# Kernel tuning notes

Hardware: AMD Instinct MI355X
Metric: run time of the kernel (lower is better)

## Reference

```python
import jax, jax.numpy as jnp
from jax import lax
import numpy as np

COST_CLASS, COST_BBOX, COST_GIOU = 2.0, 5.0, 2.0
ALPHA, GAMMA, OTA_K = 0.25, 2.0, 5
EXPANDED_STRIDES = 32.0
DEG = 180.0 / np.pi


def _make_corners(key, prefix):
    k1, k2, k3, k4, k5 = jax.random.split(key, 5)
    cx = jax.random.uniform(k1, prefix, minval=0.0, maxval=512.0)
    cy = jax.random.uniform(k2, prefix, minval=0.0, maxval=512.0)
    w = jax.random.uniform(k3, prefix, minval=8.0, maxval=128.0)
    h = jax.random.uniform(k4, prefix, minval=8.0, maxval=128.0)
    ang = jax.random.uniform(k5, prefix, minval=0.0, maxval=np.pi)
    offs = jnp.array([[-0.5, -0.5], [0.5, -0.5], [0.5, 0.5], [-0.5, 0.5]], jnp.float32)
    wh = jnp.stack([w, h], -1)[..., None, :]          # [..., 1, 2]
    pts = offs * wh                                    # [..., 4, 2]
    c, s = jnp.cos(ang)[..., None], jnp.sin(ang)[..., None]
    rx = pts[..., 0] * c - pts[..., 1] * s + cx[..., None]
    ry = pts[..., 0] * s + pts[..., 1] * c + cy[..., None]
    return jnp.stack([rx, ry], -1).reshape(prefix + (8,))


def setup_inputs() -> dict:
    key = jax.random.key(0)
    k1, k2, k3, k4 = jax.random.split(key, 4)
    B, Q, G, C = 16, 4096, 128, 80
    return {
        "pred_logits": jax.random.normal(k1, (B, Q, C), jnp.float32),
        "pred_boxes": _make_corners(k2, (B, Q)),
        "gt_boxes": _make_corners(k3, (B, G)),
        "gt_labels": jax.random.randint(k4, (B, G), 0, C),
    }


def corners_to_cxcywha(c):  # [N,8] -> [N,5]
    xc = (c[:, 0] + c[:, 2] + c[:, 4] + c[:, 6]) / 4
    yc = (c[:, 1] + c[:, 3] + c[:, 5] + c[:, 7]) / 4
    w = jnp.sqrt((c[:, 0] - c[:, 2]) ** 2 + (c[:, 1] - c[:, 3]) ** 2)
    h = jnp.sqrt((c[:, 2] - c[:, 4]) ** 2 + (c[:, 3] - c[:, 5]) ** 2)
    ang = jnp.arctan2(c[:, 3] - c[:, 1], c[:, 2] - c[:, 0]) * DEG
    return jnp.stack([xc, yc, w, h, ang], 1)


def _aabb(b5):
    cx, cy, w, h = b5[:, 0], b5[:, 1], b5[:, 2], b5[:, 3]
    return jnp.stack([cx - w / 2, cy - h / 2, cx + w / 2, cy + h / 2], 1)


def pairwise_iou(b1, b2):
    a, b = _aabb(b1), _aabb(b2)
    lt = jnp.maximum(a[:, None, :2], b[None, :, :2])
    rb = jnp.minimum(a[:, None, 2:], b[None, :, 2:])
    wh = jnp.clip(rb - lt, 0.0)
    inter = wh[..., 0] * wh[..., 1]
    area1 = (a[:, 2] - a[:, 0]) * (a[:, 3] - a[:, 1])
    area2 = (b[:, 2] - b[:, 0]) * (b[:, 3] - b[:, 1])
    return inter / (area1[:, None] + area2[None, :] - inter + 1e-8)


def pairwise_diou(b1, b2):
    iou = pairwise_iou(b1, b2)
    a, b = _aabb(b1), _aabb(b2)
    enc = jnp.maximum(a[:, None, 2:], b[None, :, 2:]) - jnp.minimum(a[:, None, :2], b[None, :, :2])
    c2 = (enc ** 2).sum(-1) + 1e-8
    d2 = ((b1[:, None, :2] - b2[None, :, :2]) ** 2).sum(-1)
    return iou - d2 / c2


def get_in_boxes_info(boxes, gts):
    bc = boxes.reshape(-1, 4, 2).mean(1)   # [Q,2]
    gp = gts.reshape(-1, 4, 2)             # [G,4,2]
    gc = gp.mean(1)                        # [G,2]
    cdist = jnp.sqrt(((bc[:, None] - gc[None]) ** 2).sum(-1))  # [Q,G]
    v1 = gp[:, 1] - gp[:, 0]
    v2 = gp[:, 2] - gp[:, 0]
    gt_area = jnp.abs(v1[:, 0] * v2[:, 1] - v1[:, 1] * v2[:, 0]) / 2
    diag = jnp.sqrt(((gp.max(1) - gp.min(1)) ** 2).sum(-1))
    radius = diag / EXPANDED_STRIDES
    in_boxes = cdist <= (gt_area / radius)[None, :]
    in_centers = cdist <= radius[None, :]
    return in_boxes.any(1), in_boxes & in_centers


def _dedup(cost, m):
    multi = m.sum(1) > 1
    onehot = jax.nn.one_hot(jnp.argmin(cost, 1), cost.shape[1], dtype=m.dtype)
    return jnp.where(multi[:, None], onehot, m)


def _match_single(logits, pboxes, gboxes, glabels):
    Q, G = pboxes.shape[0], gboxes.shape[0]
    prob = jax.nn.sigmoid(logits)
    fg_mask, _ = get_in_boxes_info(pboxes, gboxes)
    p5, g5 = corners_to_cxcywha(pboxes), corners_to_cxcywha(gboxes)
    ious = pairwise_iou(p5, g5)
    neg = (1 - ALPHA) * prob ** GAMMA * -jnp.log(1 - prob + 1e-8)
    pos = ALPHA * (1 - prob) ** GAMMA * -jnp.log(prob + 1e-8)
    cost_class = (pos - neg)[:, glabels]                         # [Q,G]
    cost_bbox = jnp.abs(pboxes[:, None] - gboxes[None]).sum(-1)  # L1 cdist on corners
    cost_giou = -pairwise_diou(p5, g5)
    # NB: source has `+ self.cost_giou * -cost_giou`, i.e. +w*diou; replicated verbatim.
    cost = COST_BBOX * cost_bbox + COST_CLASS * cost_class + COST_GIOU * (-cost_giou)
    cost = cost + 10000.0 * (~fg_mask)[:, None].astype(cost.dtype)
    # dynamic-k: sum of top OTA_K ious per gt, truncated to int, min 1
    topk = lax.top_k(ious.T, OTA_K)[0]                 # [G, k]
    dyn_k = jnp.clip(topk.sum(-1).astype(jnp.int32), 1, Q)
    ranks = jnp.argsort(jnp.argsort(cost, axis=0), axis=0)  # ascending-cost rank per column
    matching = (ranks < dyn_k[None, :]).astype(cost.dtype)
    matching = _dedup(cost, matching)
    # ensure every gt matched (bounded replication of the while loop)
    def cond(carry):
        c, m, it = carry
        return jnp.any(m.sum(0) == 0) & (it < G)
    def body(carry):
        c, m, it = carry
        c = c + 100000.0 * (m.sum(1) > 0)[:, None].astype(c.dtype)
        unm = m.sum(0) == 0
        amin = jnp.argmin(c, 0)                          # [G]
        hit = (jnp.arange(Q)[:, None] == amin[None, :]) & unm[None, :]
        m = jnp.where(hit, 1.0, m)
        m = _dedup(c, m)
        return (c, m, it + 1)
    _, matching, _ = lax.while_loop(cond, body, (cost, matching, jnp.int32(0)))
    return matching, cost, ious


def reference(pred_logits, pred_boxes, gt_boxes, gt_labels):
    return jax.vmap(_match_single)(pred_logits, pred_boxes, gt_boxes, gt_labels)
```

## Files before the change

kernel.cpp:

```cpp
#include <hip/hip_runtime.h>
#include <cstdint>
#include <cstddef>

#define B_ 16
#define Q_ 4096
#define G_ 128
#define C_ 80
#define QCHUNK 16
#define QBLK 64
#define CHPB (QBLK / QCHUNK)
#define NCH (Q_ / QBLK)

typedef unsigned long long u64;
#define U64MAX 0xffffffffffffffffull

__device__ __forceinline__ u64 packkey(float v, int q) {
    unsigned int bts = __float_as_uint(v);
    if (bts == 0x80000000u) bts = 0u;
    bts = (bts & 0x80000000u) ? ~bts : (bts | 0x80000000u);
    return ((u64)bts << 32) | (unsigned int)q;
}

__device__ __forceinline__ u64 umin64(u64 a, u64 b) { return a < b ? a : b; }
__device__ __forceinline__ u64 umax64(u64 a, u64 b) { return a > b ? a : b; }

__device__ __forceinline__ void merge5_desc(
    float& a0, float& a1, float& a2, float& a3, float& a4,
    float b0, float b1, float b2, float b3, float b4)
{
    const float r0 = fmaxf(a0, b0);
    const float r1 = fmaxf(fmaxf(a1, b1), fminf(a0, b0));
    const float r2 = fmaxf(fmaxf(a2, b2), fmaxf(fminf(a0, b1), fminf(a1, b0)));
    const float r3 = fmaxf(fmaxf(a3, b3),
                     fmaxf(fminf(a0, b2), fmaxf(fminf(a1, b1), fminf(a2, b0))));
    const float r4 = fmaxf(fmaxf(a4, b4),
                     fmaxf(fmaxf(fminf(a0, b3), fminf(a3, b0)),
                           fmaxf(fminf(a1, b2), fminf(a2, b1))));
    a0 = r0; a1 = r1; a2 = r2; a3 = r3; a4 = r4;
}

__device__ __forceinline__ void merge5_asc(
    u64& a0, u64& a1, u64& a2, u64& a3, u64& a4,
    u64 b0, u64 b1, u64 b2, u64 b3, u64 b4)
{
    const u64 r0 = umin64(a0, b0);
    const u64 r1 = umin64(umin64(a1, b1), umax64(a0, b0));
    const u64 r2 = umin64(umin64(a2, b2), umin64(umax64(a0, b1), umax64(a1, b0)));
    const u64 r3 = umin64(umin64(a3, b3),
                   umin64(umax64(a0, b2), umin64(umax64(a1, b1), umax64(a2, b0))));
    const u64 r4 = umin64(umin64(a4, b4),
                   umin64(umin64(umax64(a0, b3), umax64(a3, b0)),
                          umin64(umax64(a1, b2), umax64(a2, b1))));
    a0 = r0; a1 = r1; a2 = r2; a3 = r3; a4 = r4;
}

__device__ __forceinline__ float focal_cost(float x) {
    float p;
    if (x >= 0.f) { const float e = expf(-x); p = 1.f / (1.f + e); }
    else          { const float e = expf(x);  p = e / (1.f + e); }
    const float pos = 0.25f * (1.f - p) * (1.f - p) * (-logf(p + 1e-8f));
    const float neg = 0.75f * p * p * (-logf(1.f - p + 1e-8f));
    return pos - neg;
}

__device__ __forceinline__ void ins_level(float& c, int& j, float& x, int& qx) {
    const bool s  = x < c;
    const float nc = s ? x : c;
    const float nx = s ? c : x;
    const int   nj = s ? qx : j;
    const int   nq = s ? j : qx;
    c = nc; x = nx; j = nj; qx = nq;
}

__global__ __launch_bounds__(256) void fused_cost_kernel(
    const float* __restrict__ logits,
    const float* __restrict__ pboxes,
    const float* __restrict__ gboxes,
    const int*   __restrict__ glabels,
    float* __restrict__ out_cost,
    float* __restrict__ out_iou,
    float* __restrict__ piou,
    u64*   __restrict__ pcost,
    int*   __restrict__ ramin,
    int*   __restrict__ cnt)
{
    const int tid = threadIdx.x;
    const int g   = tid & 127;
    const int qh  = tid >> 7;
    const int ci  = blockIdx.x, b = blockIdx.y;

    __shared__ float pq[QCHUNK][16];
    __shared__ int   fgf[QCHUNK];
    __shared__ float lbuf[QCHUNK * 80];
    __shared__ float s_cost[QCHUNK][G_ + 1];
    __shared__ u64   khalf[G_][5];
    __shared__ float phalf[G_][5];

    if (tid < QBLK) cnt[b * Q_ + ci * QBLK + tid] = 0;

    const float4* gb4 = (const float4*)(gboxes + ((size_t)b * G_ + g) * 8);
    const float4 gA = gb4[0], gB = gb4[1];
    const float g0 = gA.x, g1 = gA.y, g2 = gA.z, g3 = gA.w;
    const float g4 = gB.x, g5 = gB.y, g6 = gB.z, g7 = gB.w;
    const float gxc = (g0 + g2 + g4 + g6) * 0.25f;
    const float gyc = (g1 + g3 + g5 + g7) * 0.25f;
    const float gw = sqrtf((g0 - g2) * (g0 - g2) + (g1 - g3) * (g1 - g3));
    const float gh = sqrtf((g2 - g4) * (g2 - g4) + (g3 - g5) * (g3 - g5));
    const float gax0 = gxc - gw * 0.5f, gay0 = gyc - gh * 0.5f;
    const float gax1 = gxc + gw * 0.5f, gay1 = gyc + gh * 0.5f;
    const float garea = (gax1 - gax0) * (gay1 - gay0);
    const float v1x = g2 - g0, v1y = g3 - g1, v2x = g4 - g0, v2y = g5 - g1;
    const float gt_area = fabsf(v1x * v2y - v1y * v2x) * 0.5f;
    const float mxx = fmaxf(fmaxf(g0, g2), fmaxf(g4, g6));
    const float mnx = fminf(fminf(g0, g2), fminf(g4, g6));
    const float mxy = fmaxf(fmaxf(g1, g3), fmaxf(g5, g7));
    const float mny = fminf(fminf(g1, g3), fminf(g5, g7));
    const float dgx = mxx - mnx, dgy = mxy - mny;
    const float radius = sqrtf(dgx * dgx + dgy * dgy) / 32.0f;
    const float thresh = gt_area / radius;
    const int lab = glabels[b * G_ + g];

    float c0 = 1e38f, c1 = 1e38f, c2 = 1e38f, c3 = 1e38f, c4 = 1e38f;
    int   j0 = 0, j1 = 0, j2 = 0, j3 = 0, j4 = 0;
    float t0 = 0.f, t1 = 0.f, t2 = 0.f, t3 = 0.f, t4 = 0.f;

    #pragma unroll 1
    for (int ch = 0; ch < CHPB; ++ch) {
        const int q0 = ci * QBLK + ch * QCHUNK;

        if (tid < 32) {
            const float4 v = ((const float4*)(pboxes + ((size_t)b * Q_ + q0) * 8))[tid];
            *(float4*)&pq[tid >> 1][(tid & 1) * 4] = v;
        }
        __syncthreads();
        if (tid < QCHUNK) {
            const float* pr = pq[tid];
            const float p0 = pr[0], p1 = pr[1], p2 = pr[2], p3 = pr[3];
            const float p4 = pr[4], p5v = pr[5], p6 = pr[6], p7 = pr[7];
            const float pxc = (p0 + p2 + p4 + p6) * 0.25f;
            const float pyc = (p1 + p3 + p5v + p7) * 0.25f;
            const float pw = sqrtf((p0 - p2) * (p0 - p2) + (p1 - p3) * (p1 - p3));
            const float ph = sqrtf((p2 - p4) * (p2 - p4) + (p3 - p5v) * (p3 - p5v));
            pq[tid][8]  = pxc;
            pq[tid][9]  = pyc;
            pq[tid][10] = pxc - pw * 0.5f;
            pq[tid][11] = pyc - ph * 0.5f;
            pq[tid][12] = pxc + pw * 0.5f;
            pq[tid][13] = pyc + ph * 0.5f;
            pq[tid][14] = pw * ph;
            fgf[tid] = 0;
        }
        __syncthreads();
        for (int j = tid; j < QCHUNK * 80; j += 256)
            lbuf[j] = focal_cost(logits[((size_t)b * Q_ + q0) * 80 + j]);

        const int lane0 = ((tid & 63) == 0);
        for (int i = 0; i < QCHUNK / 2; ++i) {
            const int ql = 2 * i + qh;
            const float dx = pq[ql][8] - gxc, dy = pq[ql][9] - gyc;
            const int in = sqrtf(dx * dx + dy * dy) <= thresh;
            const int anyin = __any(in);
            if (anyin && lane0) fgf[ql] = 1;
        }
        __syncthreads();

        int o = (b * Q_ + q0 + qh) * G_ + g;
        #pragma unroll
        for (int jj = 0; jj < 8; ++jj) {
            const int qls = 2 * jj + qh;
            const int q   = q0 + qls;
            const float4 prA = *(const float4*)&pq[qls][0];
            const float4 prB = *(const float4*)&pq[qls][4];
            const float4 prC = *(const float4*)&pq[qls][8];
            const float4 prD = *(const float4*)&pq[qls][12];
            const float p0 = prA.x, p1 = prA.y, p2 = prA.z, p3 = prA.w;
            const float p4 = prB.x, p5v = prB.y, p6 = prB.z, p7 = prB.w;
            const float pxc = prC.x, pyc = prC.y;
            const float pax0 = prC.z, pay0 = prC.w, pax1 = prD.x, pay1 = prD.y;
            const float parea = prD.z;

            const float l1 = fabsf(p0 - g0) + fabsf(p1 - g1) + fabsf(p2 - g2)
                           + fabsf(p3 - g3) + fabsf(p4 - g4) + fabsf(p5v - g5)
                           + fabsf(p6 - g6) + fabsf(p7 - g7);

            const float ltx = fmaxf(pax0, gax0), lty = fmaxf(pay0, gay0);
            const float rbx = fminf(pax1, gax1), rby = fminf(pay1, gay1);
            const float iw = fmaxf(rbx - ltx, 0.f), ih = fmaxf(rby - lty, 0.f);
            const float inter = iw * ih;
            const float iou = inter / (parea + garea - inter + 1e-8f);

            const float ew = fmaxf(pax1, gax1) - fminf(pax0, gax0);
            const float eh = fmaxf(pay1, gay1) - fminf(pay0, gay0);
            const float cc2 = ew * ew + eh * eh + 1e-8f;
            const float dx = pxc - gxc, dy = pyc - gyc;
            const float diou = iou - (dx * dx + dy * dy) / cc2;

            const float cclass = lbuf[qls * 80 + lab];
            const float cost = 5.f * l1 + 2.f * cclass + 2.f * diou
                             + (fgf[qls] ? 0.f : 10000.f);

            out_cost[o] = cost;
            out_iou[o]  = iou;
            o += 2 * G_;
            s_cost[qls][g] = cost;

            { float x = cost; int qx = q;
              ins_level(c0, j0, x, qx);
              ins_level(c1, j1, x, qx);
              ins_level(c2, j2, x, qx);
              ins_level(c3, j3, x, qx);
              ins_level(c4, j4, x, qx); }
            { float y = iou, m;
              m = fmaxf(t0, y); y = fminf(t0, y); t0 = m;
              m = fmaxf(t1, y); y = fminf(t1, y); t1 = m;
              m = fmaxf(t2, y); y = fminf(t2, y); t2 = m;
              m = fmaxf(t3, y); y = fminf(t3, y); t3 = m;
              t4 = fmaxf(t4, y); }
        }
        __syncthreads();

        {
            const int part = tid & 15;
            const int row  = tid >> 4;
            float v = 1e38f; int mg = 0x7fffffff;
            #pragma unroll
            for (int j = 0; j < 8; ++j) {
                const int gg = part + 16 * j;
                const float c = s_cost[row][gg];
                if (c < v) { v = c; mg = gg; }
            }
            #pragma unroll
            for (int off = 1; off < 16; off <<= 1) {
                const float ov = __shfl_xor(v, off);
                const int   og = __shfl_xor(mg, off);
                if (ov < v || (ov == v && og < mg)) { v = ov; mg = og; }
            }
            if (part == 0) ramin[b * Q_ + q0 + row] = mg;
        }
    }

    if (qh == 1) {
        khalf[g][0] = packkey(c0, j0); khalf[g][1] = packkey(c1, j1);
        khalf[g][2] = packkey(c2, j2); khalf[g][3] = packkey(c3, j3);
        khalf[g][4] = packkey(c4, j4);
        phalf[g][0] = t0; phalf[g][1] = t1; phalf[g][2] = t2;
        phalf[g][3] = t3; phalf[g][4] = t4;
    }
    __syncthreads();
    if (qh == 0) {
        u64 a0 = packkey(c0, j0), a1 = packkey(c1, j1), a2 = packkey(c2, j2),
            a3 = packkey(c3, j3), a4 = packkey(c4, j4);
        merge5_asc(a0, a1, a2, a3, a4,
                   khalf[g][0], khalf[g][1], khalf[g][2], khalf[g][3], khalf[g][4]);
        merge5_desc(t0, t1, t2, t3, t4,
                    phalf[g][0], phalf[g][1], phalf[g][2], phalf[g][3], phalf[g][4]);
        const size_t pbase = (((size_t)b * NCH + ci) * G_ + g) * 5;
        piou[pbase + 0] = t0; piou[pbase + 1] = t1; piou[pbase + 2] = t2;
        piou[pbase + 3] = t3; piou[pbase + 4] = t4;
        pcost[pbase + 0] = a0; pcost[pbase + 1] = a1; pcost[pbase + 2] = a2;
        pcost[pbase + 3] = a3; pcost[pbase + 4] = a4;
    }
}

__global__ __launch_bounds__(64) void dynk_scatter_kernel(
    const u64*   __restrict__ pcost,
    const float* __restrict__ piou,
    u64* __restrict__ cand,
    int* __restrict__ cnt,
    int* __restrict__ gsel)
{
    const int col = blockIdx.x;
    const int b = col >> 7, g = col & 127;
    const int ln = threadIdx.x;

    const size_t base = (((size_t)b * NCH + ln) * G_ + g) * 5;

    u64 k0 = pcost[base + 0], k1 = pcost[base + 1], k2 = pcost[base + 2],
        k3 = pcost[base + 3], k4 = pcost[base + 4];
    float t0 = piou[base + 0], t1 = piou[base + 1], t2 = piou[base + 2],
          t3 = piou[base + 3], t4 = piou[base + 4];

    #pragma unroll
    for (int off = 1; off < 64; off <<= 1) {
        merge5_asc(k0, k1, k2, k3, k4,
                   __shfl_xor(k0, off), __shfl_xor(k1, off), __shfl_xor(k2, off),
                   __shfl_xor(k3, off), __shfl_xor(k4, off));
        merge5_desc(t0, t1, t2, t3, t4,
                    __shfl_xor(t0, off), __shfl_xor(t1, off), __shfl_xor(t2, off),
                    __shfl_xor(t3, off), __shfl_xor(t4, off));
    }

    if (ln == 0) {
        cand[(size_t)col * 5 + 0] = k0;
        cand[(size_t)col * 5 + 1] = k1;
        cand[(size_t)col * 5 + 2] = k2;
        cand[(size_t)col * 5 + 3] = k3;
        cand[(size_t)col * 5 + 4] = k4;

        const float s = t0 + t1 + t2 + t3 + t4;
        int dynk = (int)s;
        if (dynk < 1) dynk = 1;
        if (dynk > 5) dynk = 5;
        const u64 ks[5] = {k0, k1, k2, k3, k4};
        #pragma unroll
        for (int i = 0; i < 5; ++i) {
            if (i < dynk) {
                const int q = (int)(ks[i] & 0xffffffffu);
                atomicAdd(&cnt[b * Q_ + q], 1);
                gsel[b * Q_ + q] = g;
            }
        }
    }
}

__global__ __launch_bounds__(1024) void loop_kernel(
    const float* __restrict__ cost,
    const int* __restrict__ cnt,
    const int* __restrict__ gsel,
    const int* __restrict__ ramin,
    const u64* __restrict__ cand,
    int* __restrict__ rmatch_final)
{
    const int b = blockIdx.x, tid = threadIdx.x;
    const int wv = tid >> 6, ln = tid & 63;

    __shared__ short rmatch[Q_];
    __shared__ unsigned char s_ra[Q_];
    __shared__ int newh[Q_];
    __shared__ unsigned char newg[Q_];
    __shared__ u64 scand[G_][5];
    __shared__ int ptrs[G_], col_cnt[G_], unm_list[G_], prop[G_], fb_slot[G_], touched[G_];
    __shared__ int n_unm, n_fb, n_touch;

    for (int q = tid; q < Q_; q += 1024) {
        const int c  = cnt[b * Q_ + q];
        const int ra = ramin[b * Q_ + q];
        s_ra[q] = (unsigned char)ra;
        newh[q] = 0;
        rmatch[q] = (c == 0) ? (short)-1
                             : (c == 1 ? (short)gsel[b * Q_ + q] : (short)ra);
    }
    if (tid < G_) { col_cnt[tid] = 0; ptrs[tid] = 0; }
    if (tid < G_ * 5)
        scand[tid / 5][tid % 5] = cand[(size_t)b * G_ * 5 + tid];
    __syncthreads();
    for (int q = tid; q < Q_; q += 1024)
        if (rmatch[q] >= 0) atomicAdd(&col_cnt[rmatch[q]], 1);
    __syncthreads();

    const float* costb = cost + (size_t)b * Q_ * G_;

    for (int it = 0; it < G_; ++it) {
        if (tid == 0) { n_unm = 0; n_fb = 0; n_touch = 0; }
        __syncthreads();
        if (tid < G_ && col_cnt[tid] == 0)
            unm_list[atomicAdd(&n_unm, 1)] = tid;
        __syncthreads();
        const int nu = n_unm;
        if (nu == 0) break;

        if (tid < nu) {
            const int g = unm_list[tid];
            int p = ptrs[g];
            int q = -1;
            while (p < 5) {
                const int cq = (int)(scand[g][p] & 0xffffffffu);
                if (rmatch[cq] < 0) { q = cq; break; }
                ++p;
            }
            ptrs[g] = p;
            prop[tid] = q;
            if (q < 0) fb_slot[atomicAdd(&n_fb, 1)] = tid;
        }
        __syncthreads();

        const int nf = n_fb;
        for (int i = wv; i < nf; i += 16) {
            const int slot = fb_slot[i];
            const int g = unm_list[slot];
            const float* colp = costb + g;
            u64 k0 = U64MAX, k1 = U64MAX, k2 = U64MAX, k3 = U64MAX, k4 = U64MAX;
            for (int q = ln; q < Q_; q += 64) {
                if (rmatch[q] < 0) {
                    const float v = colp[(size_t)q * G_];
                    const u64 kk = packkey(v, q);
                    if (kk < k4) {
                        if (kk < k0)      { k4 = k3; k3 = k2; k2 = k1; k1 = k0; k0 = kk; }
                        else if (kk < k1) { k4 = k3; k3 = k2; k2 = k1; k1 = kk; }
                        else if (kk < k2) { k4 = k3; k3 = k2; k2 = kk; }
                        else if (kk < k3) { k4 = k3; k3 = kk; }
                        else              { k4 = kk; }
                    }
                }
            }
            #pragma unroll
            for (int off = 1; off < 64; off <<= 1) {
                merge5_asc(k0, k1, k2, k3, k4,
                           __shfl_xor(k0, off), __shfl_xor(k1, off), __shfl_xor(k2, off),
                           __shfl_xor(k3, off), __shfl_xor(k4, off));
            }
            if (ln == 0) {
                scand[g][0] = k0; scand[g][1] = k1; scand[g][2] = k2;
                scand[g][3] = k3; scand[g][4] = k4;
                ptrs[g] = 0;
                prop[slot] = (int)(k0 & 0xffffffffu);
            }
        }
        __syncthreads();

        if (tid < nu) {
            const int q = prop[tid];
            newg[q] = (unsigned char)unm_list[tid];
            if (atomicAdd(&newh[q], 1) == 0)
                touched[atomicAdd(&n_touch, 1)] = q;
        }
        __syncthreads();

        const int nt = n_touch;
        if (tid < nt) {
            const int q = touched[tid];
            const int nh = newh[q];
            const int gg = (nh == 1) ? (int)newg[q] : (int)s_ra[q];
            rmatch[q] = (short)gg;
            atomicAdd(&col_cnt[gg], 1);
            newh[q] = 0;
        }
        __syncthreads();
    }

    for (int q = tid; q < Q_; q += 1024)
        rmatch_final[b * Q_ + q] = rmatch[q];
}

__global__ __launch_bounds__(256) void expand_kernel(
    const int* __restrict__ rmatch_final, float* __restrict__ out_match)
{
    const int idx = blockIdx.x * 256 + threadIdx.x;
    const int row = idx >> 5;
    const int gb  = (idx & 31) << 2;
    const int rm  = rmatch_final[row];
    float4 o;
    o.x = (rm == gb)     ? 1.f : 0.f;
    o.y = (rm == gb + 1) ? 1.f : 0.f;
    o.z = (rm == gb + 2) ? 1.f : 0.f;
    o.w = (rm == gb + 3) ? 1.f : 0.f;
    ((float4*)out_match)[idx] = o;
}

extern "C" void kernel_launch(void* const* d_in, const int* in_sizes, int n_in,
                              void* d_out, int out_size, void* d_ws, size_t ws_size,
                              hipStream_t stream) {
    const float* logits  = (const float*)d_in[0];
    const float* pboxes  = (const float*)d_in[1];
    const float* gboxes  = (const float*)d_in[2];
    const int*   glabels = (const int*)d_in[3];

    float* out = (float*)d_out;
    const size_t BQG = (size_t)B_ * Q_ * G_;
    float* out_match = out;
    float* out_cost  = out + BQG;
    float* out_iou   = out + 2 * BQG;

    char* ws = (char*)d_ws;
    size_t off = 0;
    u64*   pcost  = (u64*)  (ws + off); off += (size_t)B_ * NCH * G_ * 5 * 8;
    float* piou   = (float*)(ws + off); off += (size_t)B_ * NCH * G_ * 5 * 4;
    u64*   cand   = (u64*)  (ws + off); off += (size_t)B_ * G_ * 5 * 8;
    int*   ramin  = (int*)  (ws + off); off += (size_t)B_ * Q_ * 4;
    int*   cnt    = (int*)  (ws + off); off += (size_t)B_ * Q_ * 4;
    int*   gsel   = (int*)  (ws + off); off += (size_t)B_ * Q_ * 4;
    int*   rmf    = (int*)  (ws + off); off += (size_t)B_ * Q_ * 4;

    fused_cost_kernel<<<dim3(NCH, B_), 256, 0, stream>>>(
        logits, pboxes, gboxes, glabels, out_cost, out_iou, piou, pcost, ramin, cnt);
    dynk_scatter_kernel<<<B_ * G_, 64, 0, stream>>>(pcost, piou, cand, cnt, gsel);
    loop_kernel<<<B_, 1024, 0, stream>>>(out_cost, cnt, gsel, ramin, cand, rmf);
    expand_kernel<<<(int)(BQG / 4 / 256), 256, 0, stream>>>(rmf, out_match);
}
```

Before: 184.7 us.

## Hoist per-block preprocessing of boxes, logits and fg flags out of chunk loop

Loads all 64 pred boxes, focal costs and foreground flags for the block once, before the chunk loop, instead of per 16-query chunk. This cuts the number of barriers and lets the logits loads be issued together. Shared memory grows (lbuf to 64x80). To limit that growth, s_cost now shares one overlaid buffer with the khalf/phalf merge scratch, and a barrier is added at the end of each chunk iteration. The larger footprint may reduce occupancy.

```diff
diff --git a/kernel.cpp b/kernel.cpp
--- a/kernel.cpp
+++ b/kernel.cpp
@@ -88,15 +88,23 @@
     const int g   = tid & 127;
     const int qh  = tid >> 7;
     const int ci  = blockIdx.x, b = blockIdx.y;
-
-    __shared__ float pq[QCHUNK][16];
-    __shared__ int   fgf[QCHUNK];
-    __shared__ float lbuf[QCHUNK * 80];
-    __shared__ float s_cost[QCHUNK][G_ + 1];
-    __shared__ u64   khalf[G_][5];
-    __shared__ float phalf[G_][5];
-
-    if (tid < QBLK) cnt[b * Q_ + ci * QBLK + tid] = 0;
+    const int qb0 = ci * QBLK;
+
+    __shared__ float pq[QBLK][16];
+    __shared__ int   fgf[QBLK];
+    __shared__ float lbuf[QBLK * 80];
+    __shared__ __align__(16) char ovl[QCHUNK * (G_ + 1) * 4];
+    float (*s_cost)[G_ + 1] = (float(*)[G_ + 1])ovl;
+    u64   (*khalf)[5]       = (u64(*)[5])ovl;
+    float (*phalf)[5]       = (float(*)[5])(ovl + 5120);
+
+    if (tid < 128) {
+        const float4 v = ((const float4*)(pboxes + ((size_t)b * Q_ + qb0) * 8))[tid];
+        *(float4*)&pq[tid >> 1][(tid & 1) * 4] = v;
+    } else if (tid < 128 + QBLK) {
+        cnt[b * Q_ + qb0 + (tid - 128)] = 0;
+        fgf[tid - 128] = 0;
+    }
 
     const float4* gb4 = (const float4*)(gboxes + ((size_t)b * G_ + g) * 8);
     const float4 gA = gb4[0], gB = gb4[1];
@@ -120,59 +128,58 @@
     const float thresh = gt_area / radius;
     const int lab = glabels[b * G_ + g];
 
-    float c0 = 1e38f, c1 = 1e38f, c2 = 1e38f, c3 = 1e38f, c4 = 1e38f;
-    int   j0 = 0, j1 = 0, j2 = 0, j3 = 0, j4 = 0;
-    float t0 = 0.f, t1 = 0.f, t2 = 0.f, t3 = 0.f, t4 = 0.f;
-
-    #pragma unroll 1
-    for (int ch = 0; ch < CHPB; ++ch) {
-        const int q0 = ci * QBLK + ch * QCHUNK;
-
-        if (tid < 32) {
-            const float4 v = ((const float4*)(pboxes + ((size_t)b * Q_ + q0) * 8))[tid];
-            *(float4*)&pq[tid >> 1][(tid & 1) * 4] = v;
-        }
-        __syncthreads();
-        if (tid < QCHUNK) {
-            const float* pr = pq[tid];
-            const float p0 = pr[0], p1 = pr[1], p2 = pr[2], p3 = pr[3];
-            const float p4 = pr[4], p5v = pr[5], p6 = pr[6], p7 = pr[7];
-            const float pxc = (p0 + p2 + p4 + p6) * 0.25f;
-            const float pyc = (p1 + p3 + p5v + p7) * 0.25f;
-            const float pw = sqrtf((p0 - p2) * (p0 - p2) + (p1 - p3) * (p1 - p3));
-            const float ph = sqrtf((p2 - p4) * (p2 - p4) + (p3 - p5v) * (p3 - p5v));
-            pq[tid][8]  = pxc;
-            pq[tid][9]  = pyc;
-            pq[tid][10] = pxc - pw * 0.5f;
-            pq[tid][11] = pyc - ph * 0.5f;
-            pq[tid][12] = pxc + pw * 0.5f;
-            pq[tid][13] = pyc + ph * 0.5f;
-            pq[tid][14] = pw * ph;
-            fgf[tid] = 0;
-        }
-        __syncthreads();
-        for (int j = tid; j < QCHUNK * 80; j += 256)
-            lbuf[j] = focal_cost(logits[((size_t)b * Q_ + q0) * 80 + j]);
-
+    __syncthreads();
+
+    if (tid < QBLK) {
+        const float* pr = pq[tid];
+        const float p0 = pr[0], p1 = pr[1], p2 = pr[2], p3 = pr[3];
+        const float p4 = pr[4], p5v = pr[5], p6 = pr[6], p7 = pr[7];
+        const float pxc = (p0 + p2 + p4 + p6) * 0.25f;
+        const float pyc = (p1 + p3 + p5v + p7) * 0.25f;
+        const float pw = sqrtf((p0 - p2) * (p0 - p2) + (p1 - p3) * (p1 - p3));
+        const float ph = sqrtf((p2 - p4) * (p2 - p4) + (p3 - p5v) * (p3 - p5v));
+        pq[tid][8]  = pxc;
+        pq[tid][9]  = pyc;
+        pq[tid][10] = pxc - pw * 0.5f;
+        pq[tid][11] = pyc - ph * 0.5f;
+        pq[tid][12] = pxc + pw * 0.5f;
+        pq[tid][13] = pyc + ph * 0.5f;
+        pq[tid][14] = pw * ph;
+    }
+    for (int j = tid; j < QBLK * 80; j += 256)
+        lbuf[j] = focal_cost(logits[((size_t)b * Q_ + qb0) * 80 + j]);
+    __syncthreads();
+
+    {
         const int lane0 = ((tid & 63) == 0);
-        for (int i = 0; i < QCHUNK / 2; ++i) {
+        for (int i = 0; i < QBLK / 2; ++i) {
             const int ql = 2 * i + qh;
             const float dx = pq[ql][8] - gxc, dy = pq[ql][9] - gyc;
             const int in = sqrtf(dx * dx + dy * dy) <= thresh;
             const int anyin = __any(in);
             if (anyin && lane0) fgf[ql] = 1;
         }
-        __syncthreads();
+    }
+    __syncthreads();
+
+    float c0 = 1e38f, c1 = 1e38f, c2 = 1e38f, c3 = 1e38f, c4 = 1e38f;
+    int   j0 = 0, j1 = 0, j2 = 0, j3 = 0, j4 = 0;
+    float t0 = 0.f, t1 = 0.f, t2 = 0.f, t3 = 0.f, t4 = 0.f;
+
+    #pragma unroll 1
+    for (int ch = 0; ch < CHPB; ++ch) {
+        const int q0 = qb0 + ch * QCHUNK;
 
         int o = (b * Q_ + q0 + qh) * G_ + g;
         #pragma unroll
         for (int jj = 0; jj < 8; ++jj) {
-            const int qls = 2 * jj + qh;
-            const int q   = q0 + qls;
-            const float4 prA = *(const float4*)&pq[qls][0];
-            const float4 prB = *(const float4*)&pq[qls][4];
-            const float4 prC = *(const float4*)&pq[qls][8];
-            const float4 prD = *(const float4*)&pq[qls][12];
+            const int qls  = 2 * jj + qh;
+            const int qrow = ch * QCHUNK + qls;
+            const int q    = q0 + qls;
+            const float4 prA = *(const float4*)&pq[qrow][0];
+            const float4 prB = *(const float4*)&pq[qrow][4];
+            const float4 prC = *(const float4*)&pq[qrow][8];
+            const float4 prD = *(const float4*)&pq[qrow][12];
             const float p0 = prA.x, p1 = prA.y, p2 = prA.z, p3 = prA.w;
             const float p4 = prB.x, p5v = prB.y, p6 = prB.z, p7 = prB.w;
             const float pxc = prC.x, pyc = prC.y;
@@ -195,9 +202,9 @@
             const float dx = pxc - gxc, dy = pyc - gyc;
             const float diou = iou - (dx * dx + dy * dy) / cc2;
 
-            const float cclass = lbuf[qls * 80 + lab];
+            const float cclass = lbuf[qrow * 80 + lab];
             const float cost = 5.f * l1 + 2.f * cclass + 2.f * diou
-                             + (fgf[qls] ? 0.f : 10000.f);
+                             + (fgf[qrow] ? 0.f : 10000.f);
 
             out_cost[o] = cost;
             out_iou[o]  = iou;
@@ -237,6 +244,7 @@
             }
             if (part == 0) ramin[b * Q_ + q0 + row] = mg;
         }
+        __syncthreads();
     }
 
     if (qh == 1) {
```

After: 178.5 us. 3.3% less time.
